# Kernel optimization log

Hardware: AMD Instinct MI355X
Metric: run time of the kernel (lower is better)

The kernel has to match this reference:

```python
import jax, jax.numpy as jnp
import numpy as np
from jax import lax


def setup_inputs() -> dict:
    key = jax.random.key(0)
    kx, kk = jax.random.split(key)
    B, H, W, Cin, Cout, K = 32, 128, 128, 128, 128, 3
    X = jax.random.normal(kx, (B, H, W, Cin), dtype=jnp.float32)
    kernel = jax.random.normal(kk, (B, K, K, Cin, Cout), dtype=jnp.float32)
    return {"X": X, "kernel": kernel}


def reference(X, kernel):
    """Per-sample dynamic conv2d: each batch element gets its own HWIO kernel.

    Equivalent math to the TF depthwise-trick + reduce_sum, but expressed as a
    vmapped standard convolution (fuses the input-channel reduction, avoiding
    the huge [H',W',B*Cin,Cout] intermediate). Padding = 'VALID'.
    """
    dn = ('NHWC', 'HWIO', 'NHWC')

    def conv_one(x, k):
        # x: [H, W, Cin], k: [kh, kw, Cin, Cout] -> [H', W', Cout]
        return lax.conv_general_dilated(
            x[None], k, window_strides=(1, 1), padding='VALID',
            dimension_numbers=dn)[0]

    return jax.vmap(conv_one)(X, kernel)  # [B, H', W', Cout]
```

## Files before the change

kernel.cpp:

```cpp
#include <hip/hip_runtime.h>
#include <stdint.h>

typedef __attribute__((ext_vector_type(8))) short bf16x8;
typedef __attribute__((ext_vector_type(4))) float f32x4;
typedef __attribute__((ext_vector_type(4))) unsigned short u16x4;
typedef __attribute__((ext_vector_type(4))) unsigned int u32x4;

#define NB 32
#define HH 128
#define WW 128
#define CI 128
#define CO 128
#define HO 126
#define WO 126
#define TH 16
#define TW 16
#define PHh 18
#define PWw 18
#define NROW (PHh * PWw)
#define RSTR 72
#define RSTRB 144

__device__ __forceinline__ unsigned short f2bf(float f) {
  union { float f; unsigned u; } x; x.f = f;
  unsigned u = x.u;
  u += 0x7FFFu + ((u >> 16) & 1u);
  return (unsigned short)(u >> 16);
}

__device__ __forceinline__ unsigned cvtpk_bf16(float a, float b) {
  unsigned r;
  asm("v_cvt_pk_bf16_f32 %0, %1, %2" : "=v"(r) : "v"(a), "v"(b));
  return r;
}

__global__ void prep_kt(const float* __restrict__ kin, unsigned short* __restrict__ ktr) {
  __shared__ unsigned short t[CI * CO];
  int bp = blockIdx.x;
  int b = bp / 9, p = bp % 9;
  const float* src = kin + (size_t)bp * (CI * CO);
  unsigned short* dstb = ktr + (size_t)b * (9 * CI * CO);
  for (int i = threadIdx.x; i < CI * CO / 4; i += blockDim.x) {
    f32x4 v = *(const f32x4*)(src + i * 4);
    u16x4 o;
    o.x = f2bf(v.x); o.y = f2bf(v.y); o.z = f2bf(v.z); o.w = f2bf(v.w);
    *(u16x4*)&t[i * 4] = o;
  }
  __syncthreads();
  for (int j = threadIdx.x; j < 2048; j += blockDim.x) {
    int lane = j & 63, f = (j >> 6) & 7, sl = j >> 9;
    int ch = sl >> 1, kc = sl & 1;
    int co = (f >> 2) * 64 + (f & 3) * 16 + (lane & 15);
    int ci0 = ch * 64 + kc * 32 + (lane >> 4) * 8;
    bf16x8 v;
#pragma unroll
    for (int e = 0; e < 8; ++e) v[e] = t[(ci0 + e) * CO + co];
    int slice = (ch * 9 + p) * 2 + kc;
    *(bf16x8*)&dstb[(size_t)slice * 4096 + f * 512 + lane * 8] = v;
  }
}

__global__ void conv_naive(const float* __restrict__ X, const float* __restrict__ Kf,
                           float* __restrict__ out) {
  int idx = blockIdx.x * blockDim.x + threadIdx.x;
  if (idx >= NB * HO * WO * CO) return;
  int co = idx & 127, t = idx >> 7;
  int wp = t % WO; t /= WO;
  int hp = t % HO; int b = t / HO;
  const float* xb = X + (size_t)b * HH * WW * CI;
  const float* kb = Kf + (size_t)b * 9 * CI * CO;
  float s = 0.f;
  for (int p = 0; p < 9; ++p) {
    int kh = p / 3, kw = p % 3;
    const float* xr = xb + ((size_t)(hp + kh) * WW + (wp + kw)) * CI;
    const float* kr = kb + (size_t)p * CI * CO + co;
    for (int ci = 0; ci < CI; ++ci) s += xr[ci] * kr[(size_t)ci * CO];
  }
  out[idx] = s;
}

__global__ __launch_bounds__(512, 2) void conv_main(
    const float* __restrict__ X, const unsigned short* __restrict__ Kt,
    float* __restrict__ out) {
  __shared__ unsigned short lds_a[2][NROW * RSTR];

  const int tid = threadIdx.x;
  const int lane = tid & 63;
  const int wid = tid >> 6;
  const int wr = wid >> 1, wc = wid & 1;
  const int ks = lane >> 4, lr = lane & 15;

  const int bx = blockIdx.x;
  const int xcd = bx & 7, v = bx >> 3;
  const int b = xcd * 4 + (v >> 3);
  const int wt = v & 7;
  const int w0 = wt * TW;

  const float* xb = X + (size_t)b * HH * WW * CI;

  const int ci8 = tid & 7;
  unsigned okw = 0;
  int hI[6]; unsigned baseI[6];
#pragma unroll
  for (int i = 0; i < 6; ++i) {
    int row = (tid >> 3) + 64 * i;
    int h = row / PWw, w = row - PWw * h;
    int gw = w0 + w;
    if (gw < WW) okw |= (1u << i);
    hI[i] = h;
    baseI[i] = (unsigned)((h * WW + (gw & 127)) * CI + ci8 * 8);
  }
  const int dst0 = (tid >> 3) * RSTR + ci8 * 8;

  auto sIssue = [&](int i, int h0n, int chn, f32x4& ga, f32x4& gb) {
    bool live = (i < 5) | (tid < 32);
    bool ok = live && ((okw >> i) & 1) && (h0n + hI[i] < HH);
    const float* sp = xb + (ok ? baseI[i] + (unsigned)(h0n << 14) + (unsigned)(chn << 6)
                               : (unsigned)(ci8 << 3));
    ga = *(const f32x4*)sp;
    gb = *(const f32x4*)(sp + 4);
  };
  auto sWrite = [&](int i, int h0n, unsigned short* wbuf, const f32x4& ga, const f32x4& gb) {
    bool live = (i < 5) | (tid < 32);
    if (!live) return;
    bool ok = ((okw >> i) & 1) && (h0n + hI[i] < HH);
    u32x4 o;
    o.x = ok ? cvtpk_bf16(ga.x, ga.y) : 0u;
    o.y = ok ? cvtpk_bf16(ga.z, ga.w) : 0u;
    o.z = ok ? cvtpk_bf16(gb.x, gb.y) : 0u;
    o.w = ok ? cvtpk_bf16(gb.z, gb.w) : 0u;
    *(u32x4*)&wbuf[dst0 + i * 4608] = o;
  };

  const int aoff = ((wr * 4) * PWw + lr) * RSTRB + ks * 16;

  const unsigned short* ktw = Kt + (size_t)b * 9 * CI * CO + (wc * 4) * 512 + lane * 8;
  bf16x8 Hf[3][4];
  bf16x8 af[2][4];
  auto loadB = [&](bf16x8 (&dst)[4], const unsigned short* p) {
#pragma unroll
    for (int n = 0; n < 4; ++n)
      dst[n] = *(const bf16x8*)(p + n * 512);
  };
  auto issueAf = [&](bf16x8 (&dst)[4], int s, const char* rb) {
    const int kh = s / 6, jj = s % 6;
    const int kw = jj >> 1, kc = jj & 1;
#pragma unroll
    for (int m = 0; m < 4; ++m)
      dst[m] = *(const bf16x8*)(rb + aoff +
                                ((m + kh) * PWw * RSTRB + kw * RSTRB + kc * 64));
  };

  f32x4 zero = {0.f, 0.f, 0.f, 0.f};
  f32x4 acc[4][4];
#pragma unroll
  for (int m = 0; m < 4; ++m)
#pragma unroll
    for (int n = 0; n < 4; ++n) acc[m][n] = zero;
  auto mma = [&](bf16x8 (&a)[4], bf16x8 (&h)[4]) {
    __builtin_amdgcn_s_setprio(1);
#pragma unroll
    for (int m = 0; m < 4; ++m)
#pragma unroll
      for (int n = 0; n < 4; ++n)
        acc[m][n] = __builtin_amdgcn_mfma_f32_16x16x32_bf16(a[m], h[n], acc[m][n], 0, 0, 0);
    __builtin_amdgcn_s_setprio(0);
  };

  unsigned short* const A0 = &lds_a[0][0];
  unsigned short* const A1 = &lds_a[1][0];
  float* const ob = out + (size_t)b * HO * WO * CO;

  {
    f32x4 a0, b0, a1, b1, a2, b2;
    sIssue(0, 0, 0, a0, b0); sIssue(1, 0, 0, a1, b1); sIssue(2, 0, 0, a2, b2);
    sWrite(0, 0, A0, a0, b0); sWrite(1, 0, A0, a1, b1); sWrite(2, 0, A0, a2, b2);
    sIssue(3, 0, 0, a0, b0); sIssue(4, 0, 0, a1, b1); sIssue(5, 0, 0, a2, b2);
    sWrite(3, 0, A0, a0, b0); sWrite(4, 0, A0, a1, b1); sWrite(5, 0, A0, a2, b2);
  }
  loadB(Hf[0], ktw);
  loadB(Hf[1], ktw + 4096);
  __syncthreads();

  f32x4 g0a, g0b, g1a, g1b, g2a, g2b;

#pragma unroll 1
  for (int k = 0; k < 16; ++k) {
    const int ch = k & 1;
    const int h0 = (k >> 1) * TH;
    unsigned short* rbuf = ch ? A1 : A0;
    unsigned short* wbuf = ch ? A0 : A1;
    const unsigned short* bq = ktw + (size_t)ch * 73728;
    const bool stg = (k < 15);
    const int chn = (k + 1) & 1;
    const int h0n = ((k + 1) >> 1) * TH;
    const unsigned short* bqn = ktw + (size_t)chn * 73728;
    const char* rb = (const char*)rbuf;

    issueAf(af[0], 0, rb);
#pragma unroll
    for (int s = 0; s < 18; ++s) {
      if (s < 16) loadB(Hf[(s + 2) % 3], bq + (size_t)(s + 2) * 4096);
      else if (stg) loadB(Hf[(s + 2) % 3], bqn + (size_t)(s - 16) * 4096);
      if (s < 17) issueAf(af[(s + 1) & 1], s + 1, rb);
      if (stg && s == 0) {
        sIssue(0, h0n, chn, g0a, g0b);
        sIssue(1, h0n, chn, g1a, g1b);
        sIssue(2, h0n, chn, g2a, g2b);
      }
      mma(af[s & 1], Hf[s % 3]);
      if (stg && s == 5) {
        sWrite(0, h0n, wbuf, g0a, g0b);
        sWrite(1, h0n, wbuf, g1a, g1b);
        sWrite(2, h0n, wbuf, g2a, g2b);
        sIssue(3, h0n, chn, g0a, g0b);
        sIssue(4, h0n, chn, g1a, g1b);
        sIssue(5, h0n, chn, g2a, g2b);
      }
      if (stg && s == 11) {
        sWrite(3, h0n, wbuf, g0a, g0b);
        sWrite(4, h0n, wbuf, g1a, g1b);
        sWrite(5, h0n, wbuf, g2a, g2b);
      }
    }

    if (ch) {
#pragma unroll
      for (int m = 0; m < 4; ++m) {
        int hp = h0 + wr * 4 + m;
        if (hp >= HO) continue;
#pragma unroll
        for (int r = 0; r < 4; ++r) {
          int wp = w0 + ks * 4 + r;
          if (wp >= WO) continue;
#pragma unroll
          for (int n = 0; n < 4; ++n) {
            int co = wc * 64 + n * 16 + lr;
            ob[((size_t)hp * WO + wp) * CO + co] = acc[m][n][r];
          }
        }
      }
#pragma unroll
      for (int m = 0; m < 4; ++m)
#pragma unroll
        for (int n = 0; n < 4; ++n) acc[m][n] = zero;
    }
    if (k < 15) __syncthreads();
  }
}

extern "C" void kernel_launch(void* const* d_in, const int* in_sizes, int n_in,
                              void* d_out, int out_size, void* d_ws, size_t ws_size,
                              hipStream_t stream) {
  const float* X = (const float*)d_in[0];
  const float* Kf = (const float*)d_in[1];
  float* out = (float*)d_out;
  size_t need = (size_t)NB * 9 * CI * CO * sizeof(unsigned short);
  if (d_ws != nullptr && ws_size >= need) {
    unsigned short* ktr = (unsigned short*)d_ws;
    prep_kt<<<dim3(NB * 9), 256, 0, stream>>>(Kf, ktr);
    conv_main<<<dim3(256), 512, 0, stream>>>(X, ktr, out);
  } else {
    int total = NB * HO * WO * CO;
    conv_naive<<<(total + 255) / 256, 256, 0, stream>>>(X, Kf, out);
  }
}
```

Measured before the change: 188.5 us.

## Double output tile height and stage input in 32-channel quarter slices

Each block now computes a 32-row by 16-column output tile with eight accumulator rows per wave, so each weight fragment is reused across twice as many output rows. Input is staged in LDS as 32-channel quarters over a 34x18 halo instead of 64-channel halves over 18x18, which cuts the halo re-read overhead. The weight prefetch pipeline shrinks from three stages to two. This doubles accumulator register use, which at the 512-thread, two-block launch bound risks spills or lost occupancy, and each quarter now needs more sync rounds per unit of work.

```diff
diff --git a/kernel.cpp b/kernel.cpp
--- a/kernel.cpp
+++ b/kernel.cpp
@@ -13,13 +13,13 @@
 #define CO 128
 #define HO 126
 #define WO 126
-#define TH 16
+#define DTH 32
 #define TW 16
-#define PHh 18
+#define PH2 34
 #define PWw 18
-#define NROW (PHh * PWw)
-#define RSTR 72
-#define RSTRB 144
+#define NR2 (PH2 * PWw)
+#define QSH (NR2 * 32)
+#define NSLOT (NR2 * 4)
 
 __device__ __forceinline__ unsigned short f2bf(float f) {
   union { float f; unsigned u; } x; x.f = f;
@@ -82,7 +82,7 @@
 __global__ __launch_bounds__(512, 2) void conv_main(
     const float* __restrict__ X, const unsigned short* __restrict__ Kt,
     float* __restrict__ out) {
-  __shared__ unsigned short lds_a[2][NROW * RSTR];
+  __shared__ unsigned short lds_q[2][QSH];
 
   const int tid = threadIdx.x;
   const int lane = tid & 63;
@@ -98,136 +98,131 @@
 
   const float* xb = X + (size_t)b * HH * WW * CI;
 
-  const int ci8 = tid & 7;
-  unsigned okw = 0;
-  int hI[6]; unsigned baseI[6];
-#pragma unroll
-  for (int i = 0; i < 6; ++i) {
-    int row = (tid >> 3) + 64 * i;
+  const int g4 = tid & 3;
+  const int a0 = tid >> 2;
+  int hI[5]; unsigned baseI[5]; unsigned okm = 0;
+#pragma unroll
+  for (int k = 0; k < 5; ++k) {
+    int row = a0 + 128 * k;
     int h = row / PWw, w = row - PWw * h;
     int gw = w0 + w;
-    if (gw < WW) okw |= (1u << i);
-    hI[i] = h;
-    baseI[i] = (unsigned)((h * WW + (gw & 127)) * CI + ci8 * 8);
-  }
-  const int dst0 = (tid >> 3) * RSTR + ci8 * 8;
-
-  auto sIssue = [&](int i, int h0n, int chn, f32x4& ga, f32x4& gb) {
-    bool live = (i < 5) | (tid < 32);
-    bool ok = live && ((okw >> i) & 1) && (h0n + hI[i] < HH);
-    const float* sp = xb + (ok ? baseI[i] + (unsigned)(h0n << 14) + (unsigned)(chn << 6)
-                               : (unsigned)(ci8 << 3));
+    if ((row < NR2) && (gw < WW)) okm |= (1u << k);
+    hI[k] = h;
+    baseI[k] = (unsigned)((h * WW + (gw & 127)) * CI + g4 * 8);
+  }
+  const int dst0 = a0 * 32 + g4 * 8;
+
+  auto sIssue = [&](int k, int h0n, int qn, f32x4& ga, f32x4& gb) {
+    bool ok = ((okm >> k) & 1) && (h0n + hI[k] < HH);
+    const float* sp = xb + (ok ? baseI[k] + (unsigned)(h0n << 14) + (unsigned)(qn << 5)
+                               : (unsigned)(g4 * 8));
     ga = *(const f32x4*)sp;
     gb = *(const f32x4*)(sp + 4);
   };
-  auto sWrite = [&](int i, int h0n, unsigned short* wbuf, const f32x4& ga, const f32x4& gb) {
-    bool live = (i < 5) | (tid < 32);
+  auto sWrite = [&](int k, int h0n, unsigned short* wbuf, const f32x4& ga, const f32x4& gb) {
+    bool live = (k < 4) | (tid < (NSLOT - 2048));
     if (!live) return;
-    bool ok = ((okw >> i) & 1) && (h0n + hI[i] < HH);
+    bool ok = ((okm >> k) & 1) && (h0n + hI[k] < HH);
     u32x4 o;
     o.x = ok ? cvtpk_bf16(ga.x, ga.y) : 0u;
     o.y = ok ? cvtpk_bf16(ga.z, ga.w) : 0u;
     o.z = ok ? cvtpk_bf16(gb.x, gb.y) : 0u;
     o.w = ok ? cvtpk_bf16(gb.z, gb.w) : 0u;
-    *(u32x4*)&wbuf[dst0 + i * 4608] = o;
+    *(u32x4*)&wbuf[dst0 + k * 4096] = o;
   };
 
-  const int aoff = ((wr * 4) * PWw + lr) * RSTRB + ks * 16;
+  const int aoff = ((wr * 8) * PWw + lr) * 64 + ks * 16;
 
   const unsigned short* ktw = Kt + (size_t)b * 9 * CI * CO + (wc * 4) * 512 + lane * 8;
-  bf16x8 Hf[3][4];
-  bf16x8 af[2][4];
+  bf16x8 Hf[2][4];
   auto loadB = [&](bf16x8 (&dst)[4], const unsigned short* p) {
 #pragma unroll
     for (int n = 0; n < 4; ++n)
       dst[n] = *(const bf16x8*)(p + n * 512);
   };
-  auto issueAf = [&](bf16x8 (&dst)[4], int s, const char* rb) {
-    const int kh = s / 6, jj = s % 6;
-    const int kw = jj >> 1, kc = jj & 1;
-#pragma unroll
-    for (int m = 0; m < 4; ++m)
-      dst[m] = *(const bf16x8*)(rb + aoff +
-                                ((m + kh) * PWw * RSTRB + kw * RSTRB + kc * 64));
-  };
 
   f32x4 zero = {0.f, 0.f, 0.f, 0.f};
-  f32x4 acc[4][4];
-#pragma unroll
-  for (int m = 0; m < 4; ++m)
+  f32x4 acc[8][4];
+#pragma unroll
+  for (int m = 0; m < 8; ++m)
 #pragma unroll
     for (int n = 0; n < 4; ++n) acc[m][n] = zero;
-  auto mma = [&](bf16x8 (&a)[4], bf16x8 (&h)[4]) {
-    __builtin_amdgcn_s_setprio(1);
-#pragma unroll
-    for (int m = 0; m < 4; ++m)
-#pragma unroll
-      for (int n = 0; n < 4; ++n)
-        acc[m][n] = __builtin_amdgcn_mfma_f32_16x16x32_bf16(a[m], h[n], acc[m][n], 0, 0, 0);
-    __builtin_amdgcn_s_setprio(0);
-  };
-
-  unsigned short* const A0 = &lds_a[0][0];
-  unsigned short* const A1 = &lds_a[1][0];
+
   float* const ob = out + (size_t)b * HO * WO * CO;
 
   {
-    f32x4 a0, b0, a1, b1, a2, b2;
-    sIssue(0, 0, 0, a0, b0); sIssue(1, 0, 0, a1, b1); sIssue(2, 0, 0, a2, b2);
-    sWrite(0, 0, A0, a0, b0); sWrite(1, 0, A0, a1, b1); sWrite(2, 0, A0, a2, b2);
-    sIssue(3, 0, 0, a0, b0); sIssue(4, 0, 0, a1, b1); sIssue(5, 0, 0, a2, b2);
-    sWrite(3, 0, A0, a0, b0); sWrite(4, 0, A0, a1, b1); sWrite(5, 0, A0, a2, b2);
+    f32x4 ga, gb;
+#pragma unroll
+    for (int k = 0; k < 5; ++k) {
+      sIssue(k, 0, 0, ga, gb);
+      sWrite(k, 0, &lds_q[0][0], ga, gb);
+    }
   }
   loadB(Hf[0], ktw);
-  loadB(Hf[1], ktw + 4096);
   __syncthreads();
 
-  f32x4 g0a, g0b, g1a, g1b, g2a, g2b;
+  f32x4 gAa, gAb, gBa, gBb;
 
 #pragma unroll 1
   for (int k = 0; k < 16; ++k) {
-    const int ch = k & 1;
-    const int h0 = (k >> 1) * TH;
-    unsigned short* rbuf = ch ? A1 : A0;
-    unsigned short* wbuf = ch ? A0 : A1;
-    const unsigned short* bq = ktw + (size_t)ch * 73728;
+    const int q = k & 3;
+    const int h0 = (k >> 2) * DTH;
+    const char* rb = (const char*)&lds_q[k & 1][0];
+    unsigned short* wbuf = &lds_q[(k + 1) & 1][0];
+    const unsigned short* bq = ktw + (size_t)((q >> 1) * 18 + (q & 1)) * 4096;
     const bool stg = (k < 15);
-    const int chn = (k + 1) & 1;
-    const int h0n = ((k + 1) >> 1) * TH;
-    const unsigned short* bqn = ktw + (size_t)chn * 73728;
-    const char* rb = (const char*)rbuf;
-
-    issueAf(af[0], 0, rb);
-#pragma unroll
-    for (int s = 0; s < 18; ++s) {
-      if (s < 16) loadB(Hf[(s + 2) % 3], bq + (size_t)(s + 2) * 4096);
-      else if (stg) loadB(Hf[(s + 2) % 3], bqn + (size_t)(s - 16) * 4096);
-      if (s < 17) issueAf(af[(s + 1) & 1], s + 1, rb);
-      if (stg && s == 0) {
-        sIssue(0, h0n, chn, g0a, g0b);
-        sIssue(1, h0n, chn, g1a, g1b);
-        sIssue(2, h0n, chn, g2a, g2b);
+    const int qn = (k + 1) & 3;
+    const int h0n = ((k + 1) >> 2) * DTH;
+    const unsigned short* bqn = ktw + (size_t)((qn >> 1) * 18 + (qn & 1)) * 4096;
+
+#pragma unroll
+    for (int s = 0; s < 9; ++s) {
+      const int kh = s / 3, kw = s % 3;
+      if (s < 8) loadB(Hf[(s + 1) & 1], bq + (size_t)(s + 1) * 8192);
+      if (stg) {
+        if (s == 2) sWrite(0, h0n, wbuf, gAa, gAb);
+        if (s == 3) sWrite(1, h0n, wbuf, gBa, gBb);
+        if (s == 4) sWrite(2, h0n, wbuf, gAa, gAb);
+        if (s == 5) sWrite(3, h0n, wbuf, gBa, gBb);
+        if (s == 6) sWrite(4, h0n, wbuf, gAa, gAb);
+        if (s == 0) sIssue(0, h0n, qn, gAa, gAb);
+        if (s == 1) sIssue(1, h0n, qn, gBa, gBb);
+        if (s == 2) sIssue(2, h0n, qn, gAa, gAb);
+        if (s == 3) sIssue(3, h0n, qn, gBa, gBb);
+        if (s == 4) sIssue(4, h0n, qn, gAa, gAb);
       }
-      mma(af[s & 1], Hf[s % 3]);
-      if (stg && s == 5) {
-        sWrite(0, h0n, wbuf, g0a, g0b);
-        sWrite(1, h0n, wbuf, g1a, g1b);
-        sWrite(2, h0n, wbuf, g2a, g2b);
-        sIssue(3, h0n, chn, g0a, g0b);
-        sIssue(4, h0n, chn, g1a, g1b);
-        sIssue(5, h0n, chn, g2a, g2b);
+      {
+        bf16x8 af[4];
+#pragma unroll
+        for (int m = 0; m < 4; ++m)
+          af[m] = *(const bf16x8*)(rb + aoff + ((m + kh) * PWw + kw) * 64);
+        __builtin_amdgcn_s_setprio(1);
+#pragma unroll
+        for (int m = 0; m < 4; ++m)
+#pragma unroll
+          for (int n = 0; n < 4; ++n)
+            acc[m][n] = __builtin_amdgcn_mfma_f32_16x16x32_bf16(af[m], Hf[s & 1][n],
+                                                                acc[m][n], 0, 0, 0);
+        __builtin_amdgcn_s_setprio(0);
+#pragma unroll
+        for (int m = 0; m < 4; ++m)
+          af[m] = *(const bf16x8*)(rb + aoff + ((m + 4 + kh) * PWw + kw) * 64);
+        __builtin_amdgcn_s_setprio(1);
+#pragma unroll
+        for (int m = 0; m < 4; ++m)
+#pragma unroll
+          for (int n = 0; n < 4; ++n)
+            acc[m + 4][n] = __builtin_amdgcn_mfma_f32_16x16x32_bf16(af[m], Hf[s & 1][n],
+                                                                    acc[m + 4][n], 0, 0, 0);
+        __builtin_amdgcn_s_setprio(0);
       }
-      if (stg && s == 11) {
-        sWrite(3, h0n, wbuf, g0a, g0b);
-        sWrite(4, h0n, wbuf, g1a, g1b);
-        sWrite(5, h0n, wbuf, g2a, g2b);
-      }
+      if (s == 8 && stg) loadB(Hf[0], bqn);
     }
 
-    if (ch) {
-#pragma unroll
-      for (int m = 0; m < 4; ++m) {
-        int hp = h0 + wr * 4 + m;
+    if (q == 3) {
+#pragma unroll
+      for (int m = 0; m < 8; ++m) {
+        int hp = h0 + wr * 8 + m;
         if (hp >= HO) continue;
 #pragma unroll
         for (int r = 0; r < 4; ++r) {
@@ -241,7 +236,7 @@
         }
       }
 #pragma unroll
-      for (int m = 0; m < 4; ++m)
+      for (int m = 0; m < 8; ++m)
 #pragma unroll
         for (int n = 0; n < 4; ++n) acc[m][n] = zero;
     }
```

After: 183.4 us. 2.7% less time.
